# Optimization experiments

Measured on AMD Instinct MI355X. Metric: run time of the kernel, lower is better.

The kernel has to match this reference:

```python
import jax, jax.numpy as jnp
import numpy as np

N_NODES = 14   # input_size: nodes of the graph
SEQ = 24       # seq_len == GAT in/out feature dim == output_size
GAT_HID = 64
MLP_HID = 64
NEG_SLOPE = 0.2  # PyG GATConv default leaky_relu slope
B = 32768
N_EDGES = 56


def setup_inputs() -> dict:
    key = jax.random.key(0)
    ks = jax.random.split(key, 16)
    def w(k, shape, fan_in):
        return jax.random.normal(k, shape, dtype=jnp.float32) / np.sqrt(fan_in)
    return {
        "x": jax.random.normal(ks[0], (B, SEQ, N_NODES), dtype=jnp.float32),
        "edge_index": jax.random.randint(ks[1], (2, N_EDGES), 0, N_NODES, dtype=jnp.int64),
        # GATConv 1: in=24 -> out=64, heads=1
        "W1": w(ks[2], (SEQ, GAT_HID), SEQ),
        "a_src1": w(ks[3], (GAT_HID,), GAT_HID),
        "a_dst1": w(ks[4], (GAT_HID,), GAT_HID),
        "b1": jnp.zeros((GAT_HID,), dtype=jnp.float32),
        # GATConv 2: in=64 -> out=24, heads=1
        "W2": w(ks[5], (GAT_HID, SEQ), GAT_HID),
        "a_src2": w(ks[6], (SEQ,), SEQ),
        "a_dst2": w(ks[7], (SEQ,), SEQ),
        "b2": jnp.zeros((SEQ,), dtype=jnp.float32),
        # per-node 2-layer MLPs (one Linear(24,64)+ReLU+Linear(64,24) per node)
        "fc1_w": w(ks[8], (N_NODES, SEQ, MLP_HID), SEQ),
        "fc1_b": jnp.zeros((N_NODES, MLP_HID), dtype=jnp.float32),
        "fc2_w": w(ks[9], (N_NODES, MLP_HID, SEQ), MLP_HID),
        "fc2_b": jnp.zeros((N_NODES, SEQ), dtype=jnp.float32),
    }


def _gat_conv(x, src, dst, W, a_s, a_d, b):
    # PyG GATConv, heads=1, concat=False: linear -> edge attention -> edge softmax over dst -> scatter-sum
    h = x @ W                                             # [N, F]
    alpha = jax.nn.leaky_relu(h[src] @ a_s + h[dst] @ a_d, NEG_SLOPE)  # [E]
    m = jax.ops.segment_max(alpha, dst, num_segments=N_NODES)
    e = jnp.exp(alpha - m[dst])
    s = jax.ops.segment_sum(e, dst, num_segments=N_NODES)
    w = e / s[dst]
    return jax.ops.segment_sum(h[src] * w[:, None], dst, num_segments=N_NODES) + b


def reference(x, edge_index, W1, a_src1, a_dst1, b1, W2, a_src2, a_dst2, b2,
              fc1_w, fc1_b, fc2_w, fc2_b):
    ei = edge_index.astype(jnp.int32)
    loops = jnp.arange(N_NODES, dtype=jnp.int32)  # add_self_loops=True (PyG default)
    src = jnp.concatenate([ei[0], loops])
    dst = jnp.concatenate([ei[1], loops])

    def gat(xs):  # xs: [N_NODES, SEQ]
        h = jax.nn.elu(_gat_conv(xs, src, dst, W1, a_src1, a_dst1, b1))
        return _gat_conv(h, src, dst, W2, a_src2, a_dst2, b2)

    # x: [B, SEQ, N_NODES] -> transpose(1,2) -> per-sample GAT, vmapped over batch
    g = jax.vmap(gat)(x.transpose(0, 2, 1))              # [B, N_NODES, SEQ]
    # per-node 2-layer MLP, batched over nodes via einsum
    h = jax.nn.relu(jnp.einsum('bnf,nfh->bnh', g, fc1_w) + fc1_b)
    pred = jnp.einsum('bnh,nho->bno', h, fc2_w) + fc2_b  # [B, N_NODES, SEQ]
    return pred.transpose(1, 0, 2)                       # [N_NODES, B, SEQ]
```

## Files before the change

kernel.cpp:

```cpp
#include <hip/hip_runtime.h>

typedef unsigned int uu32;

#define NN 14
#define FD 24
#define HD 64
#define NE 70
#define BB 32768
#define SPW 4
#define WPB 4
#define K1_BLOCKS (BB / (WPB * SPW))
#define R2 2
#define K2_BLOCKS (NN * (BB / (256 * R2)))
#define HAP 68
#define H2P 24
#define PSZ 224

#define WSYNC() asm volatile("s_waitcnt lgkmcnt(0)" ::: "memory")

__device__ __forceinline__ float rdl(float v, int l) {
    union { float f; int i; } u;
    u.f = v;
    u.i = __builtin_amdgcn_readlane(u.i, l);
    return u.f;
}

__global__ __launch_bounds__(256) void gat_k(
    const float* __restrict__ x, const int* __restrict__ ei,
    const float* __restrict__ W1, const float* __restrict__ as1,
    const float* __restrict__ ad1, const float* __restrict__ b1,
    const float* __restrict__ W2, const float* __restrict__ as2,
    const float* __restrict__ ad2, const float* __restrict__ b2,
    float* __restrict__ Gout) {
    __shared__ __align__(16) float HA[WPB][NN * HAP];
    __shared__ __align__(16) float H2S[WPB][NN * H2P];
    __shared__ __align__(16) float PS[WPB][PSZ];
    __shared__ float sdS[WPB][2 * NN];
    __shared__ float smS[WPB][NN];
    __shared__ __align__(16) float a1S[2 * HD];
    __shared__ __align__(16) float a2S[2 * FD];
    __shared__ int esS[NE], edS[NE];

    const int tid = threadIdx.x;
    const int wv = tid >> 6;
    const int lane = tid & 63;
    float* HAw = HA[wv];
    float* H2w = H2S[wv];
    float* Pw = PS[wv];
    float* sdw = sdS[wv];
    float* smw = smS[wv];

    if (tid < 2 * HD) a1S[tid] = (tid < HD) ? as1[tid] : ad1[tid - HD];
    if (tid < 2 * FD) a2S[tid] = (tid < FD) ? as2[tid] : ad2[tid - FD];
    if (tid < 56) {
        int e64 = 1;
        for (int i = 0; i < 8; i++)
            if (ei[2 * i + 1] != 0 || (uu32)ei[2 * i] >= (uu32)NN) e64 = 0;
        esS[tid] = e64 ? ei[2 * tid] : ei[tid];
        edS[tid] = e64 ? ei[112 + 2 * tid] : ei[56 + tid];
    } else if (tid < NE) {
        esS[tid] = tid - 56;
        edS[tid] = tid - 56;
    }

    float w1r[FD];
#pragma unroll
    for (int f = 0; f < FD; f++) w1r[f] = W1[f * HD + lane];
    const float b1r = b1[lane];
    const int f2 = lane % FD;
    const int g2 = lane / FD;
    float w2r[HD];
#pragma unroll
    for (int k = 0; k < HD; k++) w2r[k] = W2[k * FD + f2];
    const float b2r = b2[f2];
    __syncthreads();
    const bool ex = (lane < NE - 64);
    const int s0 = esS[lane], d0 = edS[lane];
    const int s1 = esS[ex ? 64 + lane : 0], d1 = edS[ex ? 64 + lane : 0];

    const int gw = blockIdx.x * WPB + wv;
#pragma unroll 1
    for (int t = 0; t < SPW; t++) {
        const size_t b = (size_t)gw * SPW + t;
        const float* __restrict__ xb = x + b * (NN * FD);
        float xr[6];
        xr[0] = xb[lane];
        xr[1] = xb[64 + lane];
        xr[2] = xb[128 + lane];
        xr[3] = xb[192 + lane];
        xr[4] = xb[256 + lane];
        xr[5] = (lane < NN * FD - 320) ? xb[320 + lane] : 0.0f;
        float acc[NN];
#pragma unroll
        for (int n = 0; n < NN; n++) acc[n] = 0.0f;
#pragma unroll
        for (int f = 0; f < FD; f++) {
#pragma unroll
            for (int n = 0; n < NN; n++) {
                const int i = f * NN + n;
                acc[n] = fmaf(rdl(xr[i >> 6], i & 63), w1r[f], acc[n]);
            }
        }
#pragma unroll
        for (int n = 0; n < NN; n++) HAw[n * HAP + lane] = acc[n];
        WSYNC();
        if (lane < 2 * NN) {
            const int v = (lane >= NN) ? 1 : 0;
            const int n2 = lane - v * NN;
            float s = 0.0f;
#pragma unroll
            for (int k = 0; k < 16; k++) {
                float4 h4 = *(const float4*)&HAw[n2 * HAP + 4 * k];
                float4 a4 = *(const float4*)&a1S[v * HD + 4 * k];
                s = fmaf(h4.x, a4.x, s); s = fmaf(h4.y, a4.y, s);
                s = fmaf(h4.z, a4.z, s); s = fmaf(h4.w, a4.w, s);
            }
            sdw[v * NN + n2] = s;
        }
        if (lane < PSZ / 4)
            *(float4*)&Pw[lane * 4] = make_float4(0.f, 0.f, 0.f, 0.f);
        if (lane < NN) smw[lane] = 0.0f;
        WSYNC();
        {
            float a = sdw[s0] + sdw[NN + d0];
            a = a > 0.0f ? a : 0.2f * a;
            float e0 = __expf(a);
            atomicAdd(&smw[d0], e0);
            atomicAdd(&Pw[d0 * 16 + s0], e0);
            if (ex) {
                a = sdw[s1] + sdw[NN + d1];
                a = a > 0.0f ? a : 0.2f * a;
                float e1 = __expf(a);
                atomicAdd(&smw[d1], e1);
                atomicAdd(&Pw[d1 * 16 + s1], e1);
            }
        }
        WSYNC();
        const float pr0 = Pw[lane];
        const float pr1 = Pw[64 + lane];
        const float pr2 = Pw[128 + lane];
        const float pr3 = (lane < PSZ - 192) ? Pw[192 + lane] : 0.0f;
        const float smr = (lane < NN) ? smw[lane] : 1.0f;
        float acc2[NN];
#pragma unroll
        for (int n = 0; n < NN; n++) {
            float a = 0.0f;
#pragma unroll
            for (int k = 0; k < NN; k++) {
                const int i = n * 16 + k;
                const float pv = (i < 64) ? rdl(pr0, i) :
                                 (i < 128) ? rdl(pr1, i - 64) :
                                 (i < 192) ? rdl(pr2, i - 128) :
                                             rdl(pr3, i - 192);
                a = fmaf(pv, acc[k], a);
            }
            a = __fdividef(a, rdl(smr, n)) + b1r;
            acc2[n] = a > 0.0f ? a : (__expf(a) - 1.0f);
        }
#pragma unroll
        for (int n = 0; n < NN; n++) HAw[n * HAP + lane] = acc2[n];
        WSYNC();
        if (g2 < 2) {
#pragma unroll
            for (int i = 0; i < 7; i++) {
                const int n = g2 + 2 * i;
                float a = 0.0f;
#pragma unroll
                for (int k4 = 0; k4 < 16; k4++) {
                    float4 v4 = *(const float4*)&HAw[n * HAP + 4 * k4];
                    a = fmaf(v4.x, w2r[4 * k4 + 0], a);
                    a = fmaf(v4.y, w2r[4 * k4 + 1], a);
                    a = fmaf(v4.z, w2r[4 * k4 + 2], a);
                    a = fmaf(v4.w, w2r[4 * k4 + 3], a);
                }
                H2w[n * H2P + f2] = a;
            }
        }
        WSYNC();
        if (lane < 2 * NN) {
            const int v = (lane >= NN) ? 1 : 0;
            const int n2 = lane - v * NN;
            float s = 0.0f;
#pragma unroll
            for (int q = 0; q < 6; q++) {
                float4 h4 = *(const float4*)&H2w[n2 * H2P + 4 * q];
                float4 a4 = *(const float4*)&a2S[v * FD + 4 * q];
                s = fmaf(h4.x, a4.x, s); s = fmaf(h4.y, a4.y, s);
                s = fmaf(h4.z, a4.z, s); s = fmaf(h4.w, a4.w, s);
            }
            sdw[v * NN + n2] = s;
        }
        if (lane < PSZ / 4)
            *(float4*)&Pw[lane * 4] = make_float4(0.f, 0.f, 0.f, 0.f);
        if (lane < NN) smw[lane] = 0.0f;
        WSYNC();
        {
            float a = sdw[s0] + sdw[NN + d0];
            a = a > 0.0f ? a : 0.2f * a;
            float e0 = __expf(a);
            atomicAdd(&smw[d0], e0);
            atomicAdd(&Pw[d0 * 16 + s0], e0);
            if (ex) {
                a = sdw[s1] + sdw[NN + d1];
                a = a > 0.0f ? a : 0.2f * a;
                float e1 = __expf(a);
                atomicAdd(&smw[d1], e1);
                atomicAdd(&Pw[d1 * 16 + s1], e1);
            }
        }
        WSYNC();
        if (g2 < 2) {
            float h2c[NN];
#pragma unroll
            for (int k = 0; k < NN; k++) h2c[k] = H2w[k * H2P + f2];
#pragma unroll
            for (int i = 0; i < 7; i++) {
                const int n = g2 + 2 * i;
                float a = 0.0f;
#pragma unroll
                for (int k4 = 0; k4 < 3; k4++) {
                    float4 p4 = *(const float4*)&Pw[n * 16 + 4 * k4];
                    a = fmaf(p4.x, h2c[4 * k4 + 0], a);
                    a = fmaf(p4.y, h2c[4 * k4 + 1], a);
                    a = fmaf(p4.z, h2c[4 * k4 + 2], a);
                    a = fmaf(p4.w, h2c[4 * k4 + 3], a);
                }
                float4 p4 = *(const float4*)&Pw[n * 16 + 12];
                a = fmaf(p4.x, h2c[12], a);
                a = fmaf(p4.y, h2c[13], a);
                Gout[((size_t)n * BB + b) * FD + f2] =
                    __fdividef(a, smw[n]) + b2r;
            }
        }
        WSYNC();
    }
}

__global__ __launch_bounds__(256) void mlp_k(
    const float* __restrict__ fc1w, const float* __restrict__ fc1b,
    const float* __restrict__ fc2w, const float* __restrict__ fc2b,
    float* __restrict__ gio) {
    const int t = threadIdx.x;
    const int lane = t & 63;
    const int n = blockIdx.x >> 6;
    const int b0 = (blockIdx.x & 63) * 512;

    const float* __restrict__ W1n = fc1w + (size_t)n * (FD * HD);
    const float* __restrict__ W2n = fc2w + (size_t)n * (HD * FD);

    float w1c[FD], w2r[FD];
#pragma unroll
    for (int f = 0; f < FD; f++) w1c[f] = W1n[f * HD + lane];
#pragma unroll
    for (int f = 0; f < FD; f++) w2r[f] = W2n[lane * FD + f];
    const float b1r = fc1b[(size_t)n * HD + lane];
    const float b2r = (lane < FD) ? fc2b[(size_t)n * FD + lane] : 0.0f;

    const size_t base0 = ((size_t)n * BB + b0 + t) * FD;
    const size_t base1 = base0 + (size_t)256 * FD;
    float g0[FD], g1[FD], o0[FD], o1[FD];
#pragma unroll
    for (int q = 0; q < 6; q++) {
        *(float4*)&g0[4 * q] = *(const float4*)&gio[base0 + 4 * q];
        *(float4*)&g1[4 * q] = *(const float4*)&gio[base1 + 4 * q];
    }
#pragma unroll
    for (int f = 0; f < FD; f++) {
        const float bv = rdl(b2r, f);
        o0[f] = bv; o1[f] = bv;
    }

#pragma unroll 1
    for (int j4 = 0; j4 < 16; j4++) {
        float h0[4], h1[4];
#pragma unroll
        for (int u = 0; u < 4; u++) {
            const float bv = rdl(b1r, 4 * j4 + u);
            h0[u] = bv; h1[u] = bv;
        }
#pragma unroll
        for (int f = 0; f < FD; f++) {
            const float gf0 = g0[f], gf1 = g1[f];
#pragma unroll
            for (int u = 0; u < 4; u++) {
                const float w = rdl(w1c[f], 4 * j4 + u);
                h0[u] = fmaf(gf0, w, h0[u]);
                h1[u] = fmaf(gf1, w, h1[u]);
            }
        }
#pragma unroll
        for (int u = 0; u < 4; u++) {
            h0[u] = fmaxf(h0[u], 0.f);
            h1[u] = fmaxf(h1[u], 0.f);
        }
#pragma unroll
        for (int u = 0; u < 4; u++) {
            const float a0 = h0[u], a1 = h1[u];
#pragma unroll
            for (int f = 0; f < FD; f++) {
                const float w = rdl(w2r[f], 4 * j4 + u);
                o0[f] = fmaf(a0, w, o0[f]);
                o1[f] = fmaf(a1, w, o1[f]);
            }
        }
    }
#pragma unroll
    for (int q = 0; q < 6; q++) {
        *(float4*)&gio[base0 + 4 * q] = *(const float4*)&o0[4 * q];
        *(float4*)&gio[base1 + 4 * q] = *(const float4*)&o1[4 * q];
    }
}

extern "C" void kernel_launch(void* const* d_in, const int* in_sizes, int n_in,
                              void* d_out, int out_size, void* d_ws, size_t ws_size,
                              hipStream_t stream) {
    (void)in_sizes; (void)n_in; (void)out_size; (void)d_ws; (void)ws_size;
    const float* x    = (const float*)d_in[0];
    const int*   ei   = (const int*)d_in[1];
    const float* W1   = (const float*)d_in[2];
    const float* as1  = (const float*)d_in[3];
    const float* ad1  = (const float*)d_in[4];
    const float* b1   = (const float*)d_in[5];
    const float* W2   = (const float*)d_in[6];
    const float* as2  = (const float*)d_in[7];
    const float* ad2  = (const float*)d_in[8];
    const float* b2   = (const float*)d_in[9];
    const float* fc1w = (const float*)d_in[10];
    const float* fc1b = (const float*)d_in[11];
    const float* fc2w = (const float*)d_in[12];
    const float* fc2b = (const float*)d_in[13];
    float* gio = (float*)d_out;

    gat_k<<<dim3(K1_BLOCKS), dim3(256), 0, stream>>>(
        x, ei, W1, as1, ad1, b1, W2, as2, ad2, b2, gio);
    mlp_k<<<dim3(K2_BLOCKS), dim3(256), 0, stream>>>(
        fc1w, fc1b, fc2w, fc2b, gio);
}
```

Before: 367.9 us.

## Compute GAT layer-2 products in registers via readlane; simplify MLP to one sample per thread

In the GAT kernel, the second linear layer and the final attention aggregation no longer go through shared-memory staging done by a subset of lanes. Every lane now computes them from registers using readlane broadcasts, which removes LDS round trips and idle lanes at the cost of redundant computation across the wave. The MLP kernel now handles one sample per thread instead of two, with a fully unrolled hidden loop and twice as many blocks. This lowers register pressure and raises occupancy, but each block loads its weights for half as many samples.

```diff
diff --git a/kernel.cpp b/kernel.cpp
--- a/kernel.cpp
+++ b/kernel.cpp
@@ -10,8 +10,7 @@
 #define SPW 4
 #define WPB 4
 #define K1_BLOCKS (BB / (WPB * SPW))
-#define R2 2
-#define K2_BLOCKS (NN * (BB / (256 * R2)))
+#define K2_BLOCKS (NN * (BB / 256))
 #define HAP 68
 #define H2P 24
 #define PSZ 224
@@ -157,24 +156,18 @@
             a = __fdividef(a, rdl(smr, n)) + b1r;
             acc2[n] = a > 0.0f ? a : (__expf(a) - 1.0f);
         }
-#pragma unroll
-        for (int n = 0; n < NN; n++) HAw[n * HAP + lane] = acc2[n];
-        WSYNC();
-        if (g2 < 2) {
-#pragma unroll
-            for (int i = 0; i < 7; i++) {
-                const int n = g2 + 2 * i;
-                float a = 0.0f;
-#pragma unroll
-                for (int k4 = 0; k4 < 16; k4++) {
-                    float4 v4 = *(const float4*)&HAw[n * HAP + 4 * k4];
-                    a = fmaf(v4.x, w2r[4 * k4 + 0], a);
-                    a = fmaf(v4.y, w2r[4 * k4 + 1], a);
-                    a = fmaf(v4.z, w2r[4 * k4 + 2], a);
-                    a = fmaf(v4.w, w2r[4 * k4 + 3], a);
-                }
-                H2w[n * H2P + f2] = a;
-            }
+        float h2f[NN];
+#pragma unroll
+        for (int n = 0; n < NN; n++) h2f[n] = 0.0f;
+#pragma unroll
+        for (int k = 0; k < HD; k++) {
+#pragma unroll
+            for (int n = 0; n < NN; n++)
+                h2f[n] = fmaf(rdl(acc2[n], k), w2r[k], h2f[n]);
+        }
+        if (lane < FD) {
+#pragma unroll
+            for (int n = 0; n < NN; n++) H2w[n * H2P + lane] = h2f[n];
         }
         WSYNC();
         if (lane < 2 * NN) {
@@ -209,27 +202,35 @@
             }
         }
         WSYNC();
-        if (g2 < 2) {
-            float h2c[NN];
-#pragma unroll
-            for (int k = 0; k < NN; k++) h2c[k] = H2w[k * H2P + f2];
-#pragma unroll
-            for (int i = 0; i < 7; i++) {
-                const int n = g2 + 2 * i;
+        {
+            const float q0 = Pw[lane];
+            const float q1 = Pw[64 + lane];
+            const float q2 = Pw[128 + lane];
+            const float q3 = (lane < PSZ - 192) ? Pw[192 + lane] : 0.0f;
+            const float sr = (lane < NN) ? smw[lane] : 1.0f;
+            float gv[NN];
+#pragma unroll
+            for (int n = 0; n < NN; n++) {
                 float a = 0.0f;
 #pragma unroll
-                for (int k4 = 0; k4 < 3; k4++) {
-                    float4 p4 = *(const float4*)&Pw[n * 16 + 4 * k4];
-                    a = fmaf(p4.x, h2c[4 * k4 + 0], a);
-                    a = fmaf(p4.y, h2c[4 * k4 + 1], a);
-                    a = fmaf(p4.z, h2c[4 * k4 + 2], a);
-                    a = fmaf(p4.w, h2c[4 * k4 + 3], a);
+                for (int m = 0; m < NN; m++) {
+                    const int i = n * 16 + m;
+                    const float pv = (i < 64) ? rdl(q0, i) :
+                                     (i < 128) ? rdl(q1, i - 64) :
+                                     (i < 192) ? rdl(q2, i - 128) :
+                                                 rdl(q3, i - 192);
+                    a = fmaf(pv, h2f[m], a);
                 }
-                float4 p4 = *(const float4*)&Pw[n * 16 + 12];
-                a = fmaf(p4.x, h2c[12], a);
-                a = fmaf(p4.y, h2c[13], a);
-                Gout[((size_t)n * BB + b) * FD + f2] =
-                    __fdividef(a, smw[n]) + b2r;
+                gv[n] = __fdividef(a, rdl(sr, n)) + b2r;
+            }
+            if (g2 == 0) {
+#pragma unroll
+                for (int n = 0; n < 7; n++)
+                    Gout[((size_t)n * BB + b) * FD + f2] = gv[n];
+            } else if (g2 == 1) {
+#pragma unroll
+                for (int n = 7; n < NN; n++)
+                    Gout[((size_t)n * BB + b) * FD + f2] = gv[n];
             }
         }
         WSYNC();
@@ -242,8 +243,8 @@
     float* __restrict__ gio) {
     const int t = threadIdx.x;
     const int lane = t & 63;
-    const int n = blockIdx.x >> 6;
-    const int b0 = (blockIdx.x & 63) * 512;
+    const int n = blockIdx.x >> 7;
+    const int b0 = (blockIdx.x & 127) * 256;
 
     const float* __restrict__ W1n = fc1w + (size_t)n * (FD * HD);
     const float* __restrict__ W2n = fc2w + (size_t)n * (HD * FD);
@@ -256,59 +257,28 @@
     const float b1r = fc1b[(size_t)n * HD + lane];
     const float b2r = (lane < FD) ? fc2b[(size_t)n * FD + lane] : 0.0f;
 
-    const size_t base0 = ((size_t)n * BB + b0 + t) * FD;
-    const size_t base1 = base0 + (size_t)256 * FD;
-    float g0[FD], g1[FD], o0[FD], o1[FD];
-#pragma unroll
-    for (int q = 0; q < 6; q++) {
-        *(float4*)&g0[4 * q] = *(const float4*)&gio[base0 + 4 * q];
-        *(float4*)&g1[4 * q] = *(const float4*)&gio[base1 + 4 * q];
+    const size_t base = ((size_t)n * BB + b0 + t) * FD;
+    float g[FD], o[FD];
+#pragma unroll
+    for (int q = 0; q < 6; q++)
+        *(float4*)&g[4 * q] = *(const float4*)&gio[base + 4 * q];
+#pragma unroll
+    for (int f = 0; f < FD; f++) o[f] = rdl(b2r, f);
+
+#pragma unroll
+    for (int j = 0; j < HD; j++) {
+        float h = rdl(b1r, j);
+#pragma unroll
+        for (int f = 0; f < FD; f++)
+            h = fmaf(g[f], rdl(w1c[f], j), h);
+        h = fmaxf(h, 0.0f);
+#pragma unroll
+        for (int f = 0; f < FD; f++)
+            o[f] = fmaf(h, rdl(w2r[f], j), o[f]);
     }
 #pragma unroll
-    for (int f = 0; f < FD; f++) {
-        const float bv = rdl(b2r, f);
-        o0[f] = bv; o1[f] = bv;
-    }
-
-#pragma unroll 1
-    for (int j4 = 0; j4 < 16; j4++) {
-        float h0[4], h1[4];
-#pragma unroll
-        for (int u = 0; u < 4; u++) {
-            const float bv = rdl(b1r, 4 * j4 + u);
-            h0[u] = bv; h1[u] = bv;
-        }
-#pragma unroll
-        for (int f = 0; f < FD; f++) {
-            const float gf0 = g0[f], gf1 = g1[f];
-#pragma unroll
-            for (int u = 0; u < 4; u++) {
-                const float w = rdl(w1c[f], 4 * j4 + u);
-                h0[u] = fmaf(gf0, w, h0[u]);
-                h1[u] = fmaf(gf1, w, h1[u]);
-            }
-        }
-#pragma unroll
-        for (int u = 0; u < 4; u++) {
-            h0[u] = fmaxf(h0[u], 0.f);
-            h1[u] = fmaxf(h1[u], 0.f);
-        }
-#pragma unroll
-        for (int u = 0; u < 4; u++) {
-            const float a0 = h0[u], a1 = h1[u];
-#pragma unroll
-            for (int f = 0; f < FD; f++) {
-                const float w = rdl(w2r[f], 4 * j4 + u);
-                o0[f] = fmaf(a0, w, o0[f]);
-                o1[f] = fmaf(a1, w, o1[f]);
-            }
-        }
-    }
-#pragma unroll
-    for (int q = 0; q < 6; q++) {
-        *(float4*)&gio[base0 + 4 * q] = *(const float4*)&o0[4 * q];
-        *(float4*)&gio[base1 + 4 * q] = *(const float4*)&o1[4 * q];
-    }
+    for (int q = 0; q < 6; q++)
+        *(float4*)&gio[base + 4 * q] = *(const float4*)&o[4 * q];
 }
 
 extern "C" void kernel_launch(void* const* d_in, const int* in_sizes, int n_in,
```

New measurement: 450.1 us. +22.3%, slower.

## Stage per-node MLP weights in LDS and process one sample per thread

Applied to the files above, without the earlier changes.

The per-node MLP kernel now loads that node's fc1/fc2 weights and biases into shared memory. It reads them as uniform-address float4 broadcasts, replacing the readlane broadcasts from per-lane register columns. Each thread now handles one sample instead of two, which doubles the block count and lowers register pressure. The trade is LDS reads on the inner FMA path and an extra block-level sync plus a weight load per block.

```diff
diff --git a/kernel.cpp b/kernel.cpp
--- a/kernel.cpp
+++ b/kernel.cpp
@@ -10,8 +10,7 @@
 #define SPW 4
 #define WPB 4
 #define K1_BLOCKS (BB / (WPB * SPW))
-#define R2 2
-#define K2_BLOCKS (NN * (BB / (256 * R2)))
+#define K2_BLOCKS (NN * (BB / 256))
 #define HAP 68
 #define H2P 24
 #define PSZ 224
@@ -240,75 +239,70 @@
     const float* __restrict__ fc1w, const float* __restrict__ fc1b,
     const float* __restrict__ fc2w, const float* __restrict__ fc2b,
     float* __restrict__ gio) {
+    __shared__ __align__(16) float W1L[FD * HD];
+    __shared__ __align__(16) float W2L[HD * FD];
+    __shared__ __align__(16) float B1L[HD];
+    __shared__ __align__(16) float B2L[FD];
+
     const int t = threadIdx.x;
-    const int lane = t & 63;
-    const int n = blockIdx.x >> 6;
-    const int b0 = (blockIdx.x & 63) * 512;
-
-    const float* __restrict__ W1n = fc1w + (size_t)n * (FD * HD);
-    const float* __restrict__ W2n = fc2w + (size_t)n * (HD * FD);
-
-    float w1c[FD], w2r[FD];
-#pragma unroll
-    for (int f = 0; f < FD; f++) w1c[f] = W1n[f * HD + lane];
-#pragma unroll
-    for (int f = 0; f < FD; f++) w2r[f] = W2n[lane * FD + f];
-    const float b1r = fc1b[(size_t)n * HD + lane];
-    const float b2r = (lane < FD) ? fc2b[(size_t)n * FD + lane] : 0.0f;
-
-    const size_t base0 = ((size_t)n * BB + b0 + t) * FD;
-    const size_t base1 = base0 + (size_t)256 * FD;
-    float g0[FD], g1[FD], o0[FD], o1[FD];
+    const int n = blockIdx.x >> 7;
+    const int b0 = (blockIdx.x & 127) * 256;
+
+    const size_t base = ((size_t)n * BB + b0 + t) * FD;
+    float g[FD];
+#pragma unroll
+    for (int q = 0; q < 6; q++)
+        *(float4*)&g[4 * q] = *(const float4*)&gio[base + 4 * q];
+
+    const float4* w1p = (const float4*)(fc1w + (size_t)n * (FD * HD));
+    const float4* w2p = (const float4*)(fc2w + (size_t)n * (HD * FD));
+    for (int i = t; i < 384; i += 256) {
+        *(float4*)&W1L[4 * i] = w1p[i];
+        *(float4*)&W2L[4 * i] = w2p[i];
+    }
+    if (t < HD) B1L[t] = fc1b[n * HD + t];
+    if (t < FD) B2L[t] = fc2b[n * FD + t];
+    __syncthreads();
+
+    float o[FD];
 #pragma unroll
     for (int q = 0; q < 6; q++) {
-        *(float4*)&g0[4 * q] = *(const float4*)&gio[base0 + 4 * q];
-        *(float4*)&g1[4 * q] = *(const float4*)&gio[base1 + 4 * q];
-    }
-#pragma unroll
-    for (int f = 0; f < FD; f++) {
-        const float bv = rdl(b2r, f);
-        o0[f] = bv; o1[f] = bv;
-    }
-
-#pragma unroll 1
+        float4 b4 = *(const float4*)&B2L[4 * q];
+        o[4 * q + 0] = b4.x; o[4 * q + 1] = b4.y;
+        o[4 * q + 2] = b4.z; o[4 * q + 3] = b4.w;
+    }
+
+#pragma unroll 2
     for (int j4 = 0; j4 < 16; j4++) {
-        float h0[4], h1[4];
-#pragma unroll
-        for (int u = 0; u < 4; u++) {
-            const float bv = rdl(b1r, 4 * j4 + u);
-            h0[u] = bv; h1[u] = bv;
-        }
+        float4 b14 = *(const float4*)&B1L[4 * j4];
+        float h0 = b14.x, h1 = b14.y, h2 = b14.z, h3 = b14.w;
 #pragma unroll
         for (int f = 0; f < FD; f++) {
-            const float gf0 = g0[f], gf1 = g1[f];
-#pragma unroll
-            for (int u = 0; u < 4; u++) {
-                const float w = rdl(w1c[f], 4 * j4 + u);
-                h0[u] = fmaf(gf0, w, h0[u]);
-                h1[u] = fmaf(gf1, w, h1[u]);
-            }
-        }
-#pragma unroll
-        for (int u = 0; u < 4; u++) {
-            h0[u] = fmaxf(h0[u], 0.f);
-            h1[u] = fmaxf(h1[u], 0.f);
-        }
-#pragma unroll
-        for (int u = 0; u < 4; u++) {
-            const float a0 = h0[u], a1 = h1[u];
-#pragma unroll
-            for (int f = 0; f < FD; f++) {
-                const float w = rdl(w2r[f], 4 * j4 + u);
-                o0[f] = fmaf(a0, w, o0[f]);
-                o1[f] = fmaf(a1, w, o1[f]);
-            }
-        }
-    }
-#pragma unroll
-    for (int q = 0; q < 6; q++) {
-        *(float4*)&gio[base0 + 4 * q] = *(const float4*)&o0[4 * q];
-        *(float4*)&gio[base1 + 4 * q] = *(const float4*)&o1[4 * q];
-    }
+            float4 w4 = *(const float4*)&W1L[f * HD + 4 * j4];
+            h0 = fmaf(g[f], w4.x, h0);
+            h1 = fmaf(g[f], w4.y, h1);
+            h2 = fmaf(g[f], w4.z, h2);
+            h3 = fmaf(g[f], w4.w, h3);
+        }
+        h0 = fmaxf(h0, 0.f); h1 = fmaxf(h1, 0.f);
+        h2 = fmaxf(h2, 0.f); h3 = fmaxf(h3, 0.f);
+        float hv[4] = {h0, h1, h2, h3};
+#pragma unroll
+        for (int u2 = 0; u2 < 4; u2++) {
+            const int j = 4 * j4 + u2;
+#pragma unroll
+            for (int f4 = 0; f4 < 6; f4++) {
+                float4 w4 = *(const float4*)&W2L[j * FD + 4 * f4];
+                o[4 * f4 + 0] = fmaf(hv[u2], w4.x, o[4 * f4 + 0]);
+                o[4 * f4 + 1] = fmaf(hv[u2], w4.y, o[4 * f4 + 1]);
+                o[4 * f4 + 2] = fmaf(hv[u2], w4.z, o[4 * f4 + 2]);
+                o[4 * f4 + 3] = fmaf(hv[u2], w4.w, o[4 * f4 + 3]);
+            }
+        }
+    }
+#pragma unroll
+    for (int q = 0; q < 6; q++)
+        *(float4*)&gio[base + 4 * q] = *(const float4*)&o[4 * q];
 }
 
 extern "C" void kernel_launch(void* const* d_in, const int* in_sizes, int n_in,
```

Result: faster. 344.6 us (-6.3%).
